# Performance work log

Hardware: AMD Instinct MI355X
Metric: run time of the kernel (lower is better)

## Reference

```python
import jax, jax.numpy as jnp
import numpy as np

B_SZ, SEQ, CH, ORDER = 8, 8192, 256, 64
EPS_LN = 1e-5
EPS_H = 1e-6


def setup_inputs() -> dict:
    key = jax.random.key(0)
    ks = jax.random.split(key, 12)
    s = 1.0 / np.sqrt(CH)
    x = jax.random.normal(ks[0], (B_SZ, SEQ, CH), jnp.float32)
    # RTF params: A = denominator coeffs (monic, leading 1 implied), B = numerator coeffs
    A = 0.01 * jax.random.normal(ks[1], (CH, ORDER), jnp.float32)  # small -> stable 1/A(z)
    Bp = 0.1 * jax.random.normal(ks[2], (CH, ORDER), jnp.float32)
    h0 = jnp.zeros((1,), jnp.float32)  # init torch.tensor([0.])
    W_enc = s * jax.random.normal(ks[3], (CH, CH), jnp.float32)
    b_enc = jnp.zeros((CH,), jnp.float32)
    W_fc = s * jax.random.normal(ks[4], (CH, CH), jnp.float32)
    b_fc = jnp.zeros((CH,), jnp.float32)
    gamma = jnp.ones((CH,), jnp.float32)
    beta = jnp.zeros((CH,), jnp.float32)
    W_dec = s * jax.random.normal(ks[5], (CH, CH), jnp.float32)
    b_dec = jnp.zeros((CH,), jnp.float32)
    return {"x": x, "A": A, "Bp": Bp, "h0": h0, "W_enc": W_enc, "b_enc": b_enc,
            "W_fc": W_fc, "b_fc": b_fc, "gamma": gamma, "beta": beta,
            "W_dec": W_dec, "b_dec": b_dec}


def _rtf_kernel(A, Bp, L):
    # K(z) = B(z)/A(z) with monic denominator a = [1, A_1..A_order]
    C = A.shape[0]
    a = jnp.concatenate([jnp.ones((C, 1), A.dtype), A], axis=1)  # (C, order+1)
    af = jnp.fft.rfft(a, n=L, axis=1)
    bf = jnp.fft.rfft(Bp, n=L, axis=1)
    return jnp.fft.irfft(bf / af, n=L, axis=1)  # (C, L)


def _causal_fft_conv(x, K):
    # x: (B, L, C); K: (C, L) per-channel causal filter
    L = x.shape[1]
    n = 2 * L
    xf = jnp.fft.rfft(x, n=n, axis=1)            # (B, n/2+1, C)
    Kf = jnp.fft.rfft(K.T, n=n, axis=0)          # (n/2+1, C)
    return jnp.fft.irfft(xf * Kf[None], n=n, axis=1)[:, :L]


def reference(x, A, Bp, h0, W_enc, b_enc, W_fc, b_fc, gamma, beta, W_dec, b_dec):
    gelu = lambda t: jax.nn.gelu(t, approximate=False)
    xe = x @ W_enc.T + b_enc                      # encode
    L = xe.shape[1]
    K = _rtf_kernel(A, Bp, L)                     # kernel generation from (A,B)
    h1 = _causal_fft_conv(xe, K)                  # FFT long convolution
    y1 = gelu(h1 + h0 * xe)                       # SSMRTF output (mult_activation=gelu)
    y2 = gelu(y1 @ W_fc.T + b_fc)                 # fc + final_act
    y2 = y2 + xe                                  # skip
    mu = jnp.mean(y2, axis=-1, keepdims=True)     # LayerNorm over channels
    var = jnp.mean(jnp.square(y2 - mu), axis=-1, keepdims=True)
    y2 = (y2 - mu) * jax.lax.rsqrt(var + EPS_LN) * gamma + beta
    y = y2 @ W_dec.T + b_dec                      # decode
    # h = ||y||_inf over seq / ||x_enc||_inf over seq
    h = jnp.max(jnp.abs(y), axis=1) / (jnp.max(jnp.abs(xe), axis=1) + EPS_H)
    return (y, h)
```

## Files before the change

kernel.cpp:

```cpp
#include <hip/hip_runtime.h>
#include <math.h>


#define BSZ   8
#define SEQ   8192
#define CHN   256
#define ORD   64
#define STAPS 512
#define NDD   17
#define PREPAD 544
#define XROW  (PREPAD + SEQ)
#define MTOT  (BSZ * SEQ)
#define YELEMS (MTOT * CHN)

#define CT     2048
#define CROWE  3072

typedef short s16x8 __attribute__((ext_vector_type(8)));
typedef float f32x4 __attribute__((ext_vector_type(4)));

#define MFMA16(a, b, c) __builtin_amdgcn_mfma_f32_16x16x32_bf16((a), (b), (c), 0, 0, 0)

__device__ __forceinline__ void gll16(const void* g, void* l) {
  __builtin_amdgcn_global_load_lds(
      (const __attribute__((address_space(1))) unsigned int*)g,
      (__attribute__((address_space(3))) unsigned int*)l, 16, 0, 0);
}

#define PERMC(row, h) (((row) * 8 + ((h) ^ ((row) & 7))) * 8)

__device__ __forceinline__ unsigned short f2bf(float f) {
  unsigned u = __float_as_uint(f);
  return (unsigned short)((u + 0x7FFFu + ((u >> 16) & 1u)) >> 16);
}
__device__ __forceinline__ float bf2f(unsigned short h) {
  return __uint_as_float(((unsigned)h) << 16);
}
__device__ __forceinline__ float geluf(float x) {
  float x2 = x * x;
  float y = x * __builtin_fmaf(0.0356774081f, x2, 0.7978845608f);
  float e = __builtin_amdgcn_exp2f(-2.8853900818f * y);
  return x * __builtin_amdgcn_rcpf(1.0f + e);
}
__device__ __forceinline__ uint4 packbf8(float4 a, float4 b) {
  uint4 r;
  r.x = (unsigned)f2bf(a.x) | ((unsigned)f2bf(a.y) << 16);
  r.y = (unsigned)f2bf(a.z) | ((unsigned)f2bf(a.w) << 16);
  r.z = (unsigned)f2bf(b.x) | ((unsigned)f2bf(b.y) << 16);
  r.w = (unsigned)f2bf(b.z) | ((unsigned)f2bf(b.w) << 16);
  return r;
}

__device__ __forceinline__ void kgen8(float* smemk, const float* A, const float* Bp,
                                      unsigned short* afr, int blk) {
  int tid = threadIdx.x, lane = tid & 63, wv = tid >> 6;
  int c = blk * 8 + wv;
  float* base = smemk + wv * 1872;
  float* G0 = base;
  float* G1 = base + 584;
  float* Et = base + 1168;
  float* Asl = base + 1232;
  float* Bsl = base + 1296;
  float* Kb = base + 1360;

  Asl[lane] = A[(size_t)c * ORD + lane];
  Bsl[lane] = Bp[(size_t)c * ORD + lane];
  for (int i = lane; i < 1168; i += 64) base[i] = 0.f;
  if (lane == 0) { G0[64] = 1.f; G1[65] = 1.f; }

  for (int n = 1; n < STAPS; n <<= 1) {
    int par = (n + lane) & 1;
    const float* Gc = par ? G1 : G0;
    int I0 = 64 + n + lane + par;
    float e0 = 0.f, e1 = 0.f, e2 = 0.f, e3 = 0.f;
#pragma unroll
    for (int g = 0; g < 16; ++g) {
      float4 av = *(const float4*)&Asl[4 * g];
      float2 vA = *(const float2*)&Gc[I0 - 4 * g - 2];
      float2 vB = *(const float2*)&Gc[I0 - 4 * g - 4];
      e0 += av.x * vA.y;
      e1 += av.y * vA.x;
      e2 += av.z * vB.y;
      e3 += av.w * vB.x;
    }
    Et[lane] = (e0 + e1) + (e2 + e3);
    int nk = (n + 63) >> 6;
    for (int k = 0; k < nk; ++k) {
      int idx = k * 64 + lane;
      int parU = (idx + 1) & 1;
      const float* Gu = parU ? G1 : G0;
      int J0 = 64 + idx - 1 + parU;
      float a0 = 0.f, a1 = 0.f, a2 = 0.f, a3 = 0.f;
#pragma unroll
      for (int g = 0; g < 16; ++g) {
        float4 ev = *(const float4*)&Et[4 * g];
        float2 vA = *(const float2*)&Gu[J0 - 4 * g];
        float2 vB = *(const float2*)&Gu[J0 - 4 * g - 2];
        a0 += ev.x * vA.y;
        a1 += ev.y * vA.x;
        a2 += ev.z * vB.y;
        a3 += ev.w * vB.x;
      }
      if (idx < n) {
        float gv = -((a0 + a1) + (a2 + a3));
        G0[64 + n + idx] = gv;
        G1[65 + n + idx] = gv;
      }
    }
  }

  for (int k = 0; k < 8; ++k) {
    int t = k * 64 + lane;
    int parB = (t + 1) & 1;
    const float* Gb = parB ? G1 : G0;
    int J0 = 64 + t - 1 + parB;
    float a0 = 0.f, a1 = 0.f, a2 = 0.f, a3 = 0.f;
#pragma unroll
    for (int g = 0; g < 16; ++g) {
      float4 bv = *(const float4*)&Bsl[4 * g];
      float2 vA = *(const float2*)&Gb[J0 - 4 * g];
      float2 vB = *(const float2*)&Gb[J0 - 4 * g - 2];
      a0 += bv.x * vA.y;
      a1 += bv.y * vA.x;
      a2 += bv.z * vB.y;
      a3 += bv.w * vB.x;
    }
    Kb[t] = (a0 + a1) + (a2 + a3);
  }

  int m = lane & 15, quad = lane >> 4;
  for (int dd = 0; dd < NDD; ++dd) {
    unsigned short v[8];
#pragma unroll
    for (int j = 0; j < 8; ++j) {
      int k = quad * 8 + j;
      int d = 2 * dd + (k >> 4);
      int p = k & 15;
      int s = 16 * d + m - p;
      float kv = (s >= 0 && s < STAPS) ? Kb[s] : 0.f;
      v[j] = f2bf(kv);
    }
    uint4 pk;
    pk.x = (unsigned)v[0] | ((unsigned)v[1] << 16);
    pk.y = (unsigned)v[2] | ((unsigned)v[3] << 16);
    pk.z = (unsigned)v[4] | ((unsigned)v[5] << 16);
    pk.w = (unsigned)v[6] | ((unsigned)v[7] << 16);
    *(uint4*)(afr + ((size_t)(c * NDD + dd) * 64 + lane) * 8) = pk;
  }
}

__global__ __launch_bounds__(512) void k_pzk(const float* A, const float* Bp,
                                             unsigned short* afr,
                                             const float* we, const float* wf,
                                             const float* wd, unsigned short* owe,
                                             unsigned short* owf, unsigned short* owd,
                                             unsigned short* xeT, uint4* maxbufs) {
  __shared__ __align__(16) float smemk[8 * 1872];
  int bx = blockIdx.x, tid = threadIdx.x;
  if (bx < 32) {
    kgen8(smemk, A, Bp, afr, bx);
    return;
  }
  int i = (bx - 32) * 512 + tid;
  if (i < 196608) {
    int which = i >> 16, off = i & 65535;
    if (which == 0)      owe[off] = f2bf(we[off]);
    else if (which == 1) owf[off] = f2bf(wf[off]);
    else                 owd[off] = f2bf(wd[off]);
  } else {
    int j = i - 196608;
    uint4 z; z.x = 0; z.y = 0; z.z = 0; z.w = 0;
    if (j < 139264) {
      int row = j / 68, cc = j % 68;
      *(uint4*)((char*)xeT + (size_t)row * (XROW * 2) + (size_t)cc * 16) = z;
    } else {
      maxbufs[j - 139264] = z;
    }
  }
}

__global__ __launch_bounds__(256) void k_gemm1(const float* x, const unsigned short* wb,
                                               const float* benc, unsigned short* xeT,
                                               unsigned int* maxxe) {
  __shared__ __align__(16) unsigned short As[256 * 64];
  __shared__ __align__(16) unsigned short Bs[64 * 64];
  int tid = threadIdx.x, lane = tid & 63, wv = tid >> 6;
  int ln15 = lane & 15, hf = lane >> 4;
  size_t t0 = (size_t)blockIdx.x * 64;
  int b = (int)(t0 >> 13), tin = (int)(t0 & 8191);
  f32x4 acc[4][4];
#pragma unroll
  for (int i = 0; i < 4; ++i)
#pragma unroll
    for (int j = 0; j < 4; ++j) { acc[i][j][0]=0.f; acc[i][j][1]=0.f; acc[i][j][2]=0.f; acc[i][j][3]=0.f; }

  for (int k0 = 0; k0 < CHN; k0 += 64) {
    __syncthreads();
#pragma unroll
    for (int i = 0; i < 8; ++i) {
      int p = 512 * wv + 64 * i + lane;
      int row = p >> 3, h = (p & 7) ^ (row & 7);
      gll16(wb + (size_t)row * CHN + k0 + h * 8, &As[(512 * wv + 64 * i) * 8]);
    }
    {
      int row = tid >> 2, hb = (tid & 3) * 2;
      const float* src = x + (t0 + row) * CHN + k0 + hb * 8;
      float4 f0 = *(const float4*)src;
      float4 f1 = *(const float4*)(src + 4);
      float4 f2 = *(const float4*)(src + 8);
      float4 f3 = *(const float4*)(src + 12);
      *(uint4*)&Bs[PERMC(row, hb)]     = packbf8(f0, f1);
      *(uint4*)&Bs[PERMC(row, hb + 1)] = packbf8(f2, f3);
    }
    __syncthreads();
#pragma unroll
    for (int ks = 0; ks < 2; ++ks) {
      s16x8 af[4], bfr[4];
#pragma unroll
      for (int mt = 0; mt < 4; ++mt) {
        int row = 64 * wv + 16 * mt + ln15;
        af[mt] = *(const s16x8*)&As[PERMC(row, ks * 4 + hf)];
      }
#pragma unroll
      for (int nt = 0; nt < 4; ++nt) {
        int row = 16 * nt + ln15;
        bfr[nt] = *(const s16x8*)&Bs[PERMC(row, ks * 4 + hf)];
      }
#pragma unroll
      for (int mt = 0; mt < 4; ++mt)
#pragma unroll
        for (int nt = 0; nt < 4; ++nt)
          acc[mt][nt] = MFMA16(af[mt], bfr[nt], acc[mt][nt]);
    }
  }
  int quad = hf;
#pragma unroll
  for (int mt = 0; mt < 4; ++mt) {
#pragma unroll
    for (int r = 0; r < 4; ++r) {
      int row = 64 * wv + 16 * mt + 4 * quad + r;
      float bias = benc[row];
      float mv = 0.f;
#pragma unroll
      for (int nt = 0; nt < 4; ++nt) {
        float v = acc[mt][nt][r] + bias;
        int t = tin + 16 * nt + ln15;
        xeT[(size_t)(b * CHN + row) * XROW + PREPAD + t] = f2bf(v);
        mv = fmaxf(mv, fabsf(v));
      }
      mv = fmaxf(mv, __shfl_xor(mv, 1)); mv = fmaxf(mv, __shfl_xor(mv, 2));
      mv = fmaxf(mv, __shfl_xor(mv, 4)); mv = fmaxf(mv, __shfl_xor(mv, 8));
      if (ln15 == 0) atomicMax(&maxxe[b * CHN + row], __float_as_uint(mv));
    }
  }
}

__global__ __launch_bounds__(256) void k_conv(const unsigned short* xeT,
                                              const unsigned short* afr,
                                              unsigned short* y1, const float* h0p) {
  __shared__ __align__(16) unsigned short xet[4 * CROWE];
  __shared__ __align__(16) unsigned short bnc[4 * CT];
  int tid = threadIdx.x, lane = tid & 63, wv = tid >> 6;
  int idx = blockIdx.x;
  int tg = idx & 3, cg = (idx >> 2) & 63, b = idx >> 8;
  int c0 = cg * 4, t0 = tg * CT;
  int c = c0 + wv;

  s16x8 afrg[NDD];
  {
    const unsigned short* ap = afr + (size_t)c * (NDD * 512) + (size_t)lane * 8;
#pragma unroll
    for (int dd = 0; dd < NDD; ++dd)
      afrg[dd] = *(const s16x8*)(ap + (size_t)dd * 512);
  }
  {
    int lp = lane ^ ((lane >> 3) & 7);
    const unsigned short* gbase = xeT + (size_t)(b * CHN + c) * XROW + t0;
    unsigned short* lbase = &xet[wv * CROWE];
#pragma unroll
    for (int k = 0; k < 6; ++k)
      gll16(gbase + (size_t)(64 * k + lp) * 8, &lbase[k * 64 * 8]);
  }
  float h0 = h0p[0];

  int n = lane & 15, quad = lane >> 4;
  int qc = quad - ((quad >> 1) << 2);
  const char* xb = (const char*)&xet[wv * CROWE];

  int ad[NDD];
  {
    int cb0 = 2 * n + qc + 68;
#pragma unroll
    for (int dd = 0; dd < NDD; ++dd) {
      int cc = cb0 - 4 * dd;
      ad[dd] = (cc ^ ((cc >> 3) & 7)) * 16;
    }
  }
  int ead;
  {
    int ch = 68 + 2 * n + (quad >> 1);
    ead = (ch ^ ((ch >> 3) & 7)) * 16 + 8 * (quad & 1);
  }
  __syncthreads();

#pragma unroll 1
  for (int s = 0; s < 8; ++s) {
    f32x4 a0, a1;
    a0[0]=0.f; a0[1]=0.f; a0[2]=0.f; a0[3]=0.f;
    a1[0]=0.f; a1[1]=0.f; a1[2]=0.f; a1[3]=0.f;
#pragma unroll
    for (int dd = 0; dd < 16; dd += 2) {
      a0 = MFMA16(afrg[dd],     *(const s16x8*)(xb + ad[dd]),     a0);
      a1 = MFMA16(afrg[dd + 1], *(const s16x8*)(xb + ad[dd + 1]), a1);
    }
    a0 = MFMA16(afrg[16], *(const s16x8*)(xb + ad[16]), a0);
    uint2 xvp = *(const uint2*)(xb + ead);
    unsigned short o[4];
#pragma unroll
    for (int r = 0; r < 4; ++r) {
      float xv = bf2f(((const unsigned short*)&xvp)[r]);
      float v = (a0[r] + a1[r]) + h0 * xv;
      o[r] = f2bf(geluf(v));
    }
    uint2 pw;
    pw.x = (unsigned)o[0] | ((unsigned)o[1] << 16);
    pw.y = (unsigned)o[2] | ((unsigned)o[3] << 16);
    *(uint2*)&bnc[wv * CT + 256 * s + 16 * n + 4 * quad] = pw;
#pragma unroll
    for (int dd = 16; dd >= 8; --dd) ad[dd] = ad[dd - 8];
#pragma unroll
    for (int dd = 0; dd < 8; ++dd) ad[dd] = (ad[dd] + 512) ^ 64;
    ead = (ead + 512) ^ 64;
  }
  __syncthreads();
  {
    const size_t obase = (size_t)(b * SEQ + t0) * CHN + c0;
#pragma unroll
    for (int s = 0; s < 8; ++s) {
      int tl = 256 * s + tid;
      uint2 pk;
      pk.x = (unsigned)bnc[tl] | ((unsigned)bnc[CT + tl] << 16);
      pk.y = (unsigned)bnc[2 * CT + tl] | ((unsigned)bnc[3 * CT + tl] << 16);
      *(uint2*)(y1 + obase + (size_t)tl * CHN) = pk;
    }
  }
}

__global__ __launch_bounds__(256) void k_gemm2(const unsigned short* y1,
                                               const unsigned short* wb, const float* bfc,
                                               const unsigned short* xeT, const float* gam,
                                               const float* bet, unsigned short* y2n) {
  __shared__ __align__(16) unsigned short Ws[256 * 64];
  __shared__ __align__(16) unsigned short Asb[64 * 64];
  __shared__ float pl[64][2][2];
  int tid = threadIdx.x, lane = tid & 63, wv = tid >> 6;
  int ln15 = lane & 15, hf = lane >> 4, quad = hf;
  size_t M0 = (size_t)blockIdx.x * 64;
  int b = (int)(M0 >> 13), tin = (int)(M0 & 8191);
  int mh = wv & 1, nh = wv >> 1;
  f32x4 acc[2][8];
#pragma unroll
  for (int i = 0; i < 2; ++i)
#pragma unroll
    for (int j = 0; j < 8; ++j) { acc[i][j][0]=0.f; acc[i][j][1]=0.f; acc[i][j][2]=0.f; acc[i][j][3]=0.f; }

  for (int k0 = 0; k0 < CHN; k0 += 64) {
    __syncthreads();
#pragma unroll
    for (int i = 0; i < 8; ++i) {
      int p = 512 * wv + 64 * i + lane;
      int row = p >> 3, h = (p & 7) ^ (row & 7);
      gll16(wb + (size_t)row * CHN + k0 + h * 8, &Ws[(512 * wv + 64 * i) * 8]);
    }
#pragma unroll
    for (int i = 0; i < 2; ++i) {
      int p = 128 * wv + 64 * i + lane;
      int row = p >> 3, h = (p & 7) ^ (row & 7);
      gll16(y1 + (M0 + row) * CHN + k0 + h * 8, &Asb[(128 * wv + 64 * i) * 8]);
    }
    __syncthreads();
#pragma unroll
    for (int ks = 0; ks < 2; ++ks) {
      s16x8 af[2], bfr[8];
#pragma unroll
      for (int mt = 0; mt < 2; ++mt) {
        int row = 32 * mh + 16 * mt + ln15;
        af[mt] = *(const s16x8*)&Asb[PERMC(row, ks * 4 + hf)];
      }
#pragma unroll
      for (int nt = 0; nt < 8; ++nt) {
        int row = 128 * nh + 16 * nt + ln15;
        bfr[nt] = *(const s16x8*)&Ws[PERMC(row, ks * 4 + hf)];
      }
#pragma unroll
      for (int mt = 0; mt < 2; ++mt)
#pragma unroll
        for (int nt = 0; nt < 8; ++nt)
          acc[mt][nt] = MFMA16(af[mt], bfr[nt], acc[mt][nt]);
    }
  }
  float g8[8], be8[8], bf8[8];
#pragma unroll
  for (int nt = 0; nt < 8; ++nt) {
    int col = 128 * nh + 16 * nt + ln15;
    g8[nt] = gam[col]; be8[nt] = bet[col]; bf8[nt] = bfc[col];
  }
#pragma unroll
  for (int mt = 0; mt < 2; ++mt) {
    int mlb = 32 * mh + 16 * mt + 4 * quad;
    uint2 xv2[8];
#pragma unroll
    for (int nt = 0; nt < 8; ++nt) {
      int col = 128 * nh + 16 * nt + ln15;
      xv2[nt] = *(const uint2*)(xeT + (size_t)(b * CHN + col) * XROW + PREPAD + tin + mlb);
    }
#pragma unroll
    for (int r = 0; r < 4; ++r) {
      int ml = mlb + r;
      float s1 = 0.f, s2 = 0.f;
#pragma unroll
      for (int nt = 0; nt < 8; ++nt) {
        float t2 = acc[mt][nt][r] + bf8[nt];
        float xv = bf2f(((const unsigned short*)&xv2[nt])[r]);
        float y2 = geluf(t2) + xv;
        acc[mt][nt][r] = y2;
        s1 += y2; s2 += y2 * y2;
      }
      s1 += __shfl_xor(s1, 1); s2 += __shfl_xor(s2, 1);
      s1 += __shfl_xor(s1, 2); s2 += __shfl_xor(s2, 2);
      s1 += __shfl_xor(s1, 4); s2 += __shfl_xor(s2, 4);
      s1 += __shfl_xor(s1, 8); s2 += __shfl_xor(s2, 8);
      if (ln15 == 0) { pl[ml][nh][0] = s1; pl[ml][nh][1] = s2; }
    }
  }
  __syncthreads();
#pragma unroll
  for (int mt = 0; mt < 2; ++mt) {
#pragma unroll
    for (int r = 0; r < 4; ++r) {
      int ml = 32 * mh + 16 * mt + 4 * quad + r;
      float s1 = pl[ml][0][0] + pl[ml][1][0];
      float s2 = pl[ml][0][1] + pl[ml][1][1];
      float mu = s1 * (1.f / 256.f);
      float var = s2 * (1.f / 256.f) - mu * mu;
      float ri = rsqrtf(var + 1e-5f);
#pragma unroll
      for (int nt = 0; nt < 8; ++nt) {
        int col = 128 * nh + 16 * nt + ln15;
        float yn = (acc[mt][nt][r] - mu) * ri * g8[nt] + be8[nt];
        y2n[(M0 + ml) * CHN + col] = f2bf(yn);
      }
    }
  }
}

__global__ __launch_bounds__(256) void k_gemm3(const unsigned short* y2n,
                                               const unsigned short* wb, const float* bd,
                                               float* yout, unsigned int* maxy) {
  __shared__ __align__(16) unsigned short Ws[256 * 64];
  __shared__ __align__(16) unsigned short Asb[64 * 64];
  int tid = threadIdx.x, lane = tid & 63, wv = tid >> 6;
  int ln15 = lane & 15, hf = lane >> 4, quad = hf;
  size_t M0 = (size_t)blockIdx.x * 64;
  int b = (int)(M0 >> 13);
  int mh = wv & 1, nh = wv >> 1;
  f32x4 acc[2][8];
#pragma unroll
  for (int i = 0; i < 2; ++i)
#pragma unroll
    for (int j = 0; j < 8; ++j) { acc[i][j][0]=0.f; acc[i][j][1]=0.f; acc[i][j][2]=0.f; acc[i][j][3]=0.f; }

  for (int k0 = 0; k0 < CHN; k0 += 64) {
    __syncthreads();
#pragma unroll
    for (int i = 0; i < 8; ++i) {
      int p = 512 * wv + 64 * i + lane;
      int row = p >> 3, h = (p & 7) ^ (row & 7);
      gll16(wb + (size_t)row * CHN + k0 + h * 8, &Ws[(512 * wv + 64 * i) * 8]);
    }
#pragma unroll
    for (int i = 0; i < 2; ++i) {
      int p = 128 * wv + 64 * i + lane;
      int row = p >> 3, h = (p & 7) ^ (row & 7);
      gll16(y2n + (M0 + row) * CHN + k0 + h * 8, &Asb[(128 * wv + 64 * i) * 8]);
    }
    __syncthreads();
#pragma unroll
    for (int ks = 0; ks < 2; ++ks) {
      s16x8 af[2], bfr[8];
#pragma unroll
      for (int mt = 0; mt < 2; ++mt) {
        int row = 32 * mh + 16 * mt + ln15;
        af[mt] = *(const s16x8*)&Asb[PERMC(row, ks * 4 + hf)];
      }
#pragma unroll
      for (int nt = 0; nt < 8; ++nt) {
        int row = 128 * nh + 16 * nt + ln15;
        bfr[nt] = *(const s16x8*)&Ws[PERMC(row, ks * 4 + hf)];
      }
#pragma unroll
      for (int mt = 0; mt < 2; ++mt)
#pragma unroll
        for (int nt = 0; nt < 8; ++nt)
          acc[mt][nt] = MFMA16(af[mt], bfr[nt], acc[mt][nt]);
    }
  }
  float bd8[8];
#pragma unroll
  for (int nt = 0; nt < 8; ++nt) bd8[nt] = bd[128 * nh + 16 * nt + ln15];
#pragma unroll
  for (int mt = 0; mt < 2; ++mt)
#pragma unroll
    for (int r = 0; r < 4; ++r) {
      int ml = 32 * mh + 16 * mt + 4 * quad + r;
#pragma unroll
      for (int nt = 0; nt < 8; ++nt) {
        int col = 128 * nh + 16 * nt + ln15;
        float v = acc[mt][nt][r] + bd8[nt];
        acc[mt][nt][r] = v;
        yout[(M0 + ml) * CHN + col] = v;
      }
    }
#pragma unroll
  for (int nt = 0; nt < 8; ++nt) {
    int col = 128 * nh + 16 * nt + ln15;
    float mv = 0.f;
#pragma unroll
    for (int mt = 0; mt < 2; ++mt)
#pragma unroll
      for (int r = 0; r < 4; ++r) mv = fmaxf(mv, fabsf(acc[mt][nt][r]));
    mv = fmaxf(mv, __shfl_xor(mv, 16));
    mv = fmaxf(mv, __shfl_xor(mv, 32));
    if (quad == 0) atomicMax(&maxy[b * CHN + col], __float_as_uint(mv));
  }
}

__global__ __launch_bounds__(256) void k_hfin(const unsigned int* maxxe,
                                              const unsigned int* maxy, float* hout) {
  int i = blockIdx.x * 256 + threadIdx.x;
  if (i < BSZ * CHN) {
    float mx = __uint_as_float(maxxe[i]);
    float my = __uint_as_float(maxy[i]);
    hout[i] = my / (mx + 1e-6f);
  }
}

extern "C" void kernel_launch(void* const* d_in, const int* in_sizes, int n_in,
                              void* d_out, int out_size, void* d_ws, size_t ws_size,
                              hipStream_t stream) {
  const float* x   = (const float*)d_in[0];
  const float* A   = (const float*)d_in[1];
  const float* Bp  = (const float*)d_in[2];
  const float* h0  = (const float*)d_in[3];
  const float* We  = (const float*)d_in[4];
  const float* be  = (const float*)d_in[5];
  const float* Wf  = (const float*)d_in[6];
  const float* bfc = (const float*)d_in[7];
  const float* gam = (const float*)d_in[8];
  const float* bet = (const float*)d_in[9];
  const float* Wd  = (const float*)d_in[10];
  const float* bd  = (const float*)d_in[11];

  char* ws = (char*)d_ws;
  unsigned short* y1  = (unsigned short*)(ws + 0);
  unsigned short* afr = (unsigned short*)(ws + 33554432);
  unsigned short* web = (unsigned short*)(ws + 38010880);
  unsigned short* wfb = (unsigned short*)(ws + 38141952);
  unsigned short* wdb = (unsigned short*)(ws + 38273024);
  unsigned int*  maxxe = (unsigned int*)(ws + 38404096);
  unsigned int*  maxy  = (unsigned int*)(ws + 38412288);

  unsigned short* xeT = (unsigned short*)d_out;
  float* yout = (float*)d_out;
  float* hout = yout + YELEMS;

  k_pzk<<<690, 512, 0, stream>>>(A, Bp, afr, We, Wf, Wd, web, wfb, wdb,
                                 xeT, (uint4*)maxxe);
  k_gemm1<<<1024, 256, 0, stream>>>(x, web, be, xeT, maxxe);
  k_conv<<<2048, 256, 0, stream>>>(xeT, afr, y1, h0);
  k_gemm2<<<1024, 256, 0, stream>>>(y1, wfb, bfc, xeT, gam, bet, y1);
  k_gemm3<<<1024, 256, 0, stream>>>(y1, wdb, bd, yout, maxy);
  k_hfin<<<8, 256, 0, stream>>>(maxxe, maxy, hout);
}
```

Measured before the change: 306.7 us.

## Stage gemm1 epilogue through LDS and retile conv to 8 channels per block

The gemm1 epilogue now writes bf16 results into shared memory first, then stores them to the transposed xe buffer as 8-byte runs per row, replacing scattered 2-byte global stores. The conv kernel moves to 512 threads covering 8 channels by 1024 timesteps. This cuts the per-wave halo overhead per output and makes each output store write 8 contiguous channels instead of 4. The cost is more shared memory per block and a larger relative halo share for the shorter time tile.

```diff
diff --git a/kernel.cpp b/kernel.cpp
--- a/kernel.cpp
+++ b/kernel.cpp
@@ -13,8 +13,9 @@
 #define MTOT  (BSZ * SEQ)
 #define YELEMS (MTOT * CHN)
 
-#define CT     2048
-#define CROWE  3072
+#define CT2   1024
+#define CTP   1032
+#define CROW2 2048
 
 typedef short s16x8 __attribute__((ext_vector_type(8)));
 typedef float f32x4 __attribute__((ext_vector_type(4)));
@@ -182,8 +183,9 @@
 __global__ __launch_bounds__(256) void k_gemm1(const float* x, const unsigned short* wb,
                                                const float* benc, unsigned short* xeT,
                                                unsigned int* maxxe) {
-  __shared__ __align__(16) unsigned short As[256 * 64];
-  __shared__ __align__(16) unsigned short Bs[64 * 64];
+  __shared__ __align__(16) char smem[40960];
+  unsigned short* As = (unsigned short*)smem;
+  unsigned short* Bs = (unsigned short*)(smem + 32768);
   int tid = threadIdx.x, lane = tid & 63, wv = tid >> 6;
   int ln15 = lane & 15, hf = lane >> 4;
   size_t t0 = (size_t)blockIdx.x * 64;
@@ -234,6 +236,8 @@
     }
   }
   int quad = hf;
+  unsigned short* bb = (unsigned short*)smem;
+  __syncthreads();
 #pragma unroll
   for (int mt = 0; mt < 4; ++mt) {
 #pragma unroll
@@ -244,8 +248,7 @@
 #pragma unroll
       for (int nt = 0; nt < 4; ++nt) {
         float v = acc[mt][nt][r] + bias;
-        int t = tin + 16 * nt + ln15;
-        xeT[(size_t)(b * CHN + row) * XROW + PREPAD + t] = f2bf(v);
+        bb[row * 68 + 16 * nt + ln15] = f2bf(v);
         mv = fmaxf(mv, fabsf(v));
       }
       mv = fmaxf(mv, __shfl_xor(mv, 1)); mv = fmaxf(mv, __shfl_xor(mv, 2));
@@ -253,17 +256,27 @@
       if (ln15 == 0) atomicMax(&maxxe[b * CHN + row], __float_as_uint(mv));
     }
   }
-}
-
-__global__ __launch_bounds__(256) void k_conv(const unsigned short* xeT,
+  __syncthreads();
+  {
+    int rbase = wv * 4 + quad;
+#pragma unroll
+    for (int it = 0; it < 16; ++it) {
+      int row = it * 16 + rbase;
+      uint2 val = *(const uint2*)&bb[row * 68 + ln15 * 4];
+      *(uint2*)(xeT + (size_t)(b * CHN + row) * XROW + PREPAD + tin + ln15 * 4) = val;
+    }
+  }
+}
+
+__global__ __launch_bounds__(512) void k_conv(const unsigned short* xeT,
                                               const unsigned short* afr,
                                               unsigned short* y1, const float* h0p) {
-  __shared__ __align__(16) unsigned short xet[4 * CROWE];
-  __shared__ __align__(16) unsigned short bnc[4 * CT];
+  __shared__ __align__(16) unsigned short xet[8 * CROW2];
+  __shared__ __align__(16) unsigned short bnc[8 * CTP];
   int tid = threadIdx.x, lane = tid & 63, wv = tid >> 6;
   int idx = blockIdx.x;
-  int tg = idx & 3, cg = (idx >> 2) & 63, b = idx >> 8;
-  int c0 = cg * 4, t0 = tg * CT;
+  int tg = idx & 7, cg = (idx >> 3) & 31, b = idx >> 8;
+  int c0 = cg * 8, t0 = tg * CT2;
   int c = c0 + wv;
 
   s16x8 afrg[NDD];
@@ -276,16 +289,16 @@
   {
     int lp = lane ^ ((lane >> 3) & 7);
     const unsigned short* gbase = xeT + (size_t)(b * CHN + c) * XROW + t0;
-    unsigned short* lbase = &xet[wv * CROWE];
-#pragma unroll
-    for (int k = 0; k < 6; ++k)
+    unsigned short* lbase = &xet[wv * CROW2];
+#pragma unroll
+    for (int k = 0; k < 4; ++k)
       gll16(gbase + (size_t)(64 * k + lp) * 8, &lbase[k * 64 * 8]);
   }
   float h0 = h0p[0];
 
   int n = lane & 15, quad = lane >> 4;
   int qc = quad - ((quad >> 1) << 2);
-  const char* xb = (const char*)&xet[wv * CROWE];
+  const char* xb = (const char*)&xet[wv * CROW2];
 
   int ad[NDD];
   {
@@ -304,7 +317,7 @@
   __syncthreads();
 
 #pragma unroll 1
-  for (int s = 0; s < 8; ++s) {
+  for (int s = 0; s < 4; ++s) {
     f32x4 a0, a1;
     a0[0]=0.f; a0[1]=0.f; a0[2]=0.f; a0[3]=0.f;
     a1[0]=0.f; a1[1]=0.f; a1[2]=0.f; a1[3]=0.f;
@@ -325,7 +338,7 @@
     uint2 pw;
     pw.x = (unsigned)o[0] | ((unsigned)o[1] << 16);
     pw.y = (unsigned)o[2] | ((unsigned)o[3] << 16);
-    *(uint2*)&bnc[wv * CT + 256 * s + 16 * n + 4 * quad] = pw;
+    *(uint2*)&bnc[wv * CTP + 256 * s + 16 * n + 4 * quad] = pw;
 #pragma unroll
     for (int dd = 16; dd >= 8; --dd) ad[dd] = ad[dd - 8];
 #pragma unroll
@@ -335,13 +348,14 @@
   __syncthreads();
   {
     const size_t obase = (size_t)(b * SEQ + t0) * CHN + c0;
-#pragma unroll
-    for (int s = 0; s < 8; ++s) {
-      int tl = 256 * s + tid;
+    int tb = tid >> 1, h = (tid & 1) * 4;
+#pragma unroll
+    for (int s = 0; s < 4; ++s) {
+      int tl = 256 * s + tb;
       uint2 pk;
-      pk.x = (unsigned)bnc[tl] | ((unsigned)bnc[CT + tl] << 16);
-      pk.y = (unsigned)bnc[2 * CT + tl] | ((unsigned)bnc[3 * CT + tl] << 16);
-      *(uint2*)(y1 + obase + (size_t)tl * CHN) = pk;
+      pk.x = (unsigned)bnc[(h + 0) * CTP + tl] | ((unsigned)bnc[(h + 1) * CTP + tl] << 16);
+      pk.y = (unsigned)bnc[(h + 2) * CTP + tl] | ((unsigned)bnc[(h + 3) * CTP + tl] << 16);
+      *(uint2*)(y1 + obase + (size_t)tl * CHN + h) = pk;
     }
   }
 }
@@ -577,7 +591,7 @@
   k_pzk<<<690, 512, 0, stream>>>(A, Bp, afr, We, Wf, Wd, web, wfb, wdb,
                                  xeT, (uint4*)maxxe);
   k_gemm1<<<1024, 256, 0, stream>>>(x, web, be, xeT, maxxe);
-  k_conv<<<2048, 256, 0, stream>>>(xeT, afr, y1, h0);
+  k_conv<<<2048, 512, 0, stream>>>(xeT, afr, y1, h0);
   k_gemm2<<<1024, 256, 0, stream>>>(y1, wfb, bfc, xeT, gam, bet, y1);
   k_gemm3<<<1024, 256, 0, stream>>>(y1, wdb, bd, yout, maxy);
   k_hfin<<<8, 256, 0, stream>>>(maxxe, maxy, hout);
```

New measurement: 308.0 us. About the same (+0.4%).
